# Optimization experiments

Measured on AMD Instinct MI355X. Metric: run time of the kernel, lower is better.

The kernel has to match this reference:

```python
import jax, jax.numpy as jnp
import numpy as np

N = 262144          # pixels (512x512 image)
F = 2               # in_features (x, y)
K = 13              # num_frequencies
H = 256             # dim_hidden
OUT = 3             # out_features (RGB)
TILES = [1, 4, 16, 64, 256]   # prod(tile_dims[i]) per layer
PE_DIM = F + 2 * F * K        # 54


def setup_inputs() -> dict:
    key = jax.random.key(0)
    ks = jax.random.split(key, 2 * len(TILES) + 3)
    inp = {"coords": jax.random.uniform(ks[0], (N, F), dtype=jnp.float32)}
    d_in = PE_DIM
    for i, t in enumerate(TILES):
        # kaiming-uniform-like scale; biases init to zero as in the module
        bound = float(np.sqrt(6.0 / d_in))
        inp[f"w{i}"] = jax.random.uniform(ks[1 + i], (t, d_in, H), dtype=jnp.float32,
                                           minval=-bound, maxval=bound)
        inp[f"b{i}"] = jnp.zeros((H,), dtype=jnp.float32)
        d_in = H
    bound = float(np.sqrt(6.0 / H))
    inp["w_last"] = jax.random.uniform(ks[-1], (OUT, H), dtype=jnp.float32,
                                        minval=-bound, maxval=bound)
    inp["b_last"] = jnp.zeros((OUT,), dtype=jnp.float32)
    return inp


def _pos_enc(coords):
    # NeRF positional encoding, concat order: coords, then for each freq i,
    # for each feature j: sin(2^i * pi * c_j), cos(2^i * pi * c_j)
    freqs = (2.0 ** jnp.arange(K, dtype=jnp.float32)) * np.pi      # [K]
    ang = coords[:, None, :] * freqs[None, :, None]                # [N, K, F]
    enc = jnp.stack([jnp.sin(ang), jnp.cos(ang)], axis=-1)         # [N, K, F, 2]
    enc = enc.reshape(coords.shape[0], 2 * K * F)
    return jnp.concatenate([coords, enc], axis=-1)                 # [N, PE_DIM]


def reference(coords, w0, b0, w1, b1, w2, b2, w3, b3, w4, b4, w_last, b_last):
    x = _pos_enc(coords)                                           # [N, 54]
    for w, b in ((w0, b0), (w1, b1), (w2, b2), (w3, b3), (w4, b4)):
        t = w.shape[0]
        x = x.reshape(t, -1, x.shape[-1])                          # [T, N/T, d_in]
        x = jnp.einsum('tnd,tdo->tno', x, w) + b                   # per-tile GEMM
        x = jnp.where(x > 0, x, 0.2 * x)                           # LeakyReLU(0.2)
    x = x.reshape(-1, H)                                           # [N, H]
    return x @ w_last.T + b_last                                   # [N, OUT]
```

## Files before the change

### kernel.cpp

```cpp
#include <hip/hip_runtime.h>
#include <stdint.h>

typedef uint32_t u32;
typedef short s16x8 __attribute__((ext_vector_type(8)));
typedef float f32x16 __attribute__((ext_vector_type(16)));
typedef u32 u32x2 __attribute__((ext_vector_type(2)));
typedef u32 u32x4 __attribute__((ext_vector_type(4)));

#define NPIX   262144
#define HD     256

#define FTHR      512
#define PXB       128
#define NBLK      (NPIX / PXB)
#define ACT_LDS   65536

#define B0_OFF  0u
#define B1_OFF  32768u
#define B2_OFF  557056u
#define B3_OFF  2654208u
#define B4_OFF  11042816u
#define BH_OFF  44597248u
#define BLOB_TOTAL 44613632u
#define F_W1 2048u
#define F_W2 34816u
#define F_W3 165888u
#define F_W4 690176u
#define F_WH 2787328u
#define F_END 2788352u

#define ACT_BYTES  131072
#define WBUF_BYTES 16384
#define FB_LDS     (ACT_BYTES + 2 * WBUF_BYTES)

__device__ __forceinline__ u32 bfpair(float a, float b) {
    u32 ua = __builtin_bit_cast(u32, a);
    u32 ub = __builtin_bit_cast(u32, b);
    ua = (ua + 0x7FFFu + ((ua >> 16) & 1u)) >> 16;
    ub = (ub + 0x7FFFu + ((ub >> 16) & 1u)) >> 16;
    return ua | (ub << 16);
}
__device__ __forceinline__ u32 act_off(int row, int colByte) {
    return (u32)((row << 9) + (colByte ^ ((row & 31) << 4)));
}
__device__ __forceinline__ u32 w_off32(int col, int kByte) {
    return (u32)((col << 6) + (kByte ^ (((col >> 1) & 3) << 4)));
}

extern "C" __global__ __launch_bounds__(256)
void loe_prepass(const float* __restrict__ w0, const float* __restrict__ w1,
                 const float* __restrict__ w2, const float* __restrict__ w3,
                 const float* __restrict__ w4, const float* __restrict__ wl,
                 char* __restrict__ ws)
{
    const u32 f = blockIdx.x * 256 + threadIdx.x;
    if (f >= F_END) return;
    float v[8];
    char* dst;
    if (f < F_W1) {
        const u32 kk = f >> 9, fb = (f >> 6) & 7, lane = f & 63;
        const u32 l31 = lane & 31, lhi = lane >> 5;
        const u32 k0 = kk * 16 + lhi * 8, col = fb * 32 + l31;
        #pragma unroll
        for (int j = 0; j < 8; ++j)
            v[j] = (k0 + j < 54) ? w0[(k0 + j) * HD + col] : 0.0f;
        dst = ws + B0_OFF + (size_t)f * 16;
    } else if (f < F_WH) {
        const float* W; size_t boff; u32 fl;
        if (f < F_W2)      { W = w1; boff = B1_OFF; fl = f - F_W1; }
        else if (f < F_W3) { W = w2; boff = B2_OFF; fl = f - F_W2; }
        else if (f < F_W4) { W = w3; boff = B3_OFF; fl = f - F_W3; }
        else               { W = w4; boff = B4_OFF; fl = f - F_W4; }
        const u32 t = fl >> 13, c = fl & 8191;
        const u32 kk = c >> 9, fb = (c >> 6) & 7, lane = c & 63;
        const u32 l31 = lane & 31, lhi = lane >> 5;
        const u32 k0 = kk * 16 + lhi * 8, col = fb * 32 + l31;
        const float* src = W + (size_t)t * 65536 + (size_t)k0 * HD + col;
        #pragma unroll
        for (int j = 0; j < 8; ++j) v[j] = src[(size_t)j * HD];
        dst = ws + boff + (size_t)fl * 16;
    } else {
        const u32 fl = f - F_WH;
        const u32 kk = fl >> 6, lane = fl & 63;
        const u32 l31 = lane & 31, lhi = lane >> 5;
        const u32 k0 = kk * 16 + lhi * 8;
        #pragma unroll
        for (int j = 0; j < 8; ++j)
            v[j] = (l31 < 3) ? wl[l31 * HD + k0 + j] : 0.0f;
        dst = ws + BH_OFF + (size_t)fl * 16;
    }
    u32x4 pk;
    pk.x = bfpair(v[0], v[1]); pk.y = bfpair(v[2], v[3]);
    pk.z = bfpair(v[4], v[5]); pk.w = bfpair(v[6], v[7]);
    *reinterpret_cast<u32x4*>(dst) = pk;
}

extern "C" __global__ __launch_bounds__(FTHR, 4)
void loe_fused_pre(const float* __restrict__ coords,
                   const float* __restrict__ b0, const float* __restrict__ b1,
                   const float* __restrict__ b2, const float* __restrict__ b3,
                   const float* __restrict__ b4, const float* __restrict__ bl,
                   const char* __restrict__ blob,
                   float* __restrict__ out)
{
    extern __shared__ char lds[];

    const int tid  = threadIdx.x;
    const int lane = tid & 63;
    const int wv   = tid >> 6;
    const int l31  = lane & 31;
    const int lhi  = lane >> 5;

    const int bid  = (int)blockIdx.x;
    const int pb   = ((bid & 7) << 8) | (bid >> 3);
    const int pix0 = pb << 7;

    {
        const int p = tid >> 2;
        const int h = tid & 3;
        const float2 c2 = reinterpret_cast<const float2*>(coords)[pix0 + p];
        const float cf[2] = {c2.x, c2.y};
        #pragma unroll
        for (int u = 0; u < 16; u += 2) {
            float v[2];
            #pragma unroll
            for (int q = 0; q < 2; ++q) {
                const int c = h * 16 + u + q;
                float val;
                if (c < 2) val = cf[c];
                else if (c - 2 >= 52) val = 0.0f;
                else {
                    const int e = c - 2;
                    const float a = cf[(e >> 1) & 1] * (float)(1 << (e >> 2));
                    val = (e & 1) ? cospif(a) : sinpif(a);
                }
                v[q] = val;
            }
            *reinterpret_cast<u32*>(lds + act_off(p, (h * 16 + u) * 2)) = bfpair(v[0], v[1]);
        }
    }

    f32x16 acc[4];
    const u32 swz = (u32)(l31 << 4);
    u32 abase[4];
    #pragma unroll
    for (int pt = 0; pt < 4; ++pt) abase[pt] = (u32)((pt * 32 + l31) << 9);

    auto init_acc = [&](const float* Bias) {
        #pragma unroll
        for (int q = 0; q < 4; ++q) {
            const float4 bv = *reinterpret_cast<const float4*>(Bias + wv * 32 + q * 8 + lhi * 4);
            #pragma unroll
            for (int pt = 0; pt < 4; ++pt) {
                acc[pt][q * 4 + 0] = bv.x; acc[pt][q * 4 + 1] = bv.y;
                acc[pt][q * 4 + 2] = bv.z; acc[pt][q * 4 + 3] = bv.w;
            }
        }
    };

    auto epilogue = [&]() {
        #pragma unroll
        for (int q = 0; q < 4; ++q) {
            const int oc0 = wv * 32 + q * 8 + lhi * 4;
            #pragma unroll
            for (int pt = 0; pt < 4; ++pt) {
                float x[4];
                #pragma unroll
                for (int j = 0; j < 4; ++j) {
                    const float v = acc[pt][q * 4 + j];
                    x[j] = fmaxf(v, 0.2f * v);
                }
                u32x2 wo;
                wo.x = bfpair(x[0], x[1]);
                wo.y = bfpair(x[2], x[3]);
                *reinterpret_cast<u32x2*>(lds + act_off(pt * 32 + l31, oc0 * 2)) = wo;
            }
        }
    };

    auto run_layer = [&](int KK, const char* wbase, const float* Bias) {
        init_acc(Bias);
        __syncthreads();
        const char* f0 = wbase + (size_t)wv * 1024 + (size_t)lane * 16;
        u32x4 wA = *reinterpret_cast<const u32x4*>(f0);
        u32x4 wB = *reinterpret_cast<const u32x4*>(f0 + 8192);
        #pragma unroll 4
        for (int kk = 0; kk < KK; kk += 2) {
            const int n2 = (kk + 2 < KK) ? kk + 2 : kk;
            const int n3 = (kk + 3 < KK) ? kk + 3 : KK - 1;
            const u32x4 nA = *reinterpret_cast<const u32x4*>(f0 + (size_t)n2 * 8192);
            const u32x4 nB = *reinterpret_cast<const u32x4*>(f0 + (size_t)n3 * 8192);
            {
                const u32 cb = (u32)(kk * 32 + lhi * 16) ^ swz;
                s16x8 af[4];
                #pragma unroll
                for (int pt = 0; pt < 4; ++pt)
                    af[pt] = *reinterpret_cast<const s16x8*>(lds + abase[pt] + cb);
                const s16x8 a = __builtin_bit_cast(s16x8, wA);
                #pragma unroll
                for (int pt = 0; pt < 4; ++pt)
                    acc[pt] = __builtin_amdgcn_mfma_f32_32x32x16_bf16(a, af[pt], acc[pt], 0, 0, 0);
            }
            {
                const u32 cb = (u32)((kk + 1) * 32 + lhi * 16) ^ swz;
                s16x8 af[4];
                #pragma unroll
                for (int pt = 0; pt < 4; ++pt)
                    af[pt] = *reinterpret_cast<const s16x8*>(lds + abase[pt] + cb);
                const s16x8 a = __builtin_bit_cast(s16x8, wB);
                #pragma unroll
                for (int pt = 0; pt < 4; ++pt)
                    acc[pt] = __builtin_amdgcn_mfma_f32_32x32x16_bf16(a, af[pt], acc[pt], 0, 0, 0);
            }
            wA = nA; wB = nB;
        }
        __syncthreads();
        epilogue();
    };

    const char* b0p = blob + B0_OFF;
    const char* b1p = blob + B1_OFF + (size_t)(pb >> 9) * 131072;
    const char* b2p = blob + B2_OFF + (size_t)(pb >> 7) * 131072;
    const char* b3p = blob + B3_OFF + (size_t)(pb >> 5) * 131072;
    const char* b4p = blob + B4_OFF + (size_t)(pb >> 3) * 131072;
    const char* bHp = blob + BH_OFF;

    run_layer(4,  b0p, b0);
    run_layer(16, b1p, b1);
    run_layer(16, b2p, b2);
    run_layer(16, b3p, b3);
    run_layer(16, b4p, b4);

    __syncthreads();
    if (wv < 4) {
        f32x16 a;
        #pragma unroll
        for (int r = 0; r < 16; ++r) a[r] = 0.0f;
        const u32 hrow = (u32)((wv * 32 + l31) << 9);
        #pragma unroll 4
        for (int kk = 0; kk < 16; ++kk) {
            const u32x4 wh = *reinterpret_cast<const u32x4*>(bHp + (size_t)kk * 1024 + (size_t)lane * 16);
            const u32 cb = (u32)(kk * 32 + lhi * 16) ^ swz;
            const s16x8 af = *reinterpret_cast<const s16x8*>(lds + hrow + cb);
            a = __builtin_amdgcn_mfma_f32_32x32x16_bf16(__builtin_bit_cast(s16x8, wh), af, a, 0, 0, 0);
        }
        if (lhi == 0) {
            const int p = pix0 + wv * 32 + l31;
            out[p * 3 + 0] = a[0] + bl[0];
            out[p * 3 + 1] = a[1] + bl[1];
            out[p * 3 + 2] = a[2] + bl[2];
        }
    }
}

extern "C" __global__ __launch_bounds__(512, 2)
void loe_fused_fb(const float* __restrict__ coords,
                  const float* __restrict__ w0, const float* __restrict__ b0,
                  const float* __restrict__ w1, const float* __restrict__ b1,
                  const float* __restrict__ w2, const float* __restrict__ b2,
                  const float* __restrict__ w3, const float* __restrict__ b3,
                  const float* __restrict__ w4, const float* __restrict__ b4,
                  const float* __restrict__ wl, const float* __restrict__ bl,
                  float* __restrict__ out)
{
    extern __shared__ char lds[];
    const int tid  = threadIdx.x;
    const int lane = tid & 63;
    const int wv   = tid >> 6;
    const int wr   = wv >> 2;
    const int wc   = wv & 3;
    const int l31  = lane & 31;
    const int lhi  = lane >> 5;
    const int bid  = (int)blockIdx.x;
    const int pb   = ((bid & 7) << 7) | (bid >> 3);
    const int pix0 = pb << 8;
    const int scol = tid & 255;
    const int kh   = tid >> 8;

    float st[16];
    auto load_plain = [&](const float* W, int s) {
        const float* src = W + (size_t)(s * 32 + kh * 16) * HD + scol;
        #pragma unroll
        for (int j = 0; j < 16; ++j) st[j] = src[(size_t)j * HD];
    };
    auto load_guard = [&](const float* W, int s) {
        #pragma unroll
        for (int j = 0; j < 16; ++j) {
            const int k = s * 32 + kh * 16 + j;
            st[j] = (k < 54) ? W[k * HD + scol] : 0.0f;
        }
    };
    load_guard(w0, 0);
    {
        const int p = tid >> 1;
        const int h = tid & 1;
        const float2 c2 = reinterpret_cast<const float2*>(coords)[pix0 + p];
        const float cf[2] = {c2.x, c2.y};
        #pragma unroll
        for (int u = 0; u < 32; u += 2) {
            float v[2];
            #pragma unroll
            for (int q = 0; q < 2; ++q) {
                const int c = h * 32 + u + q;
                float val;
                if (c < 2) val = cf[c];
                else if (c - 2 >= 52) val = 0.0f;
                else {
                    const int e = c - 2;
                    const float a = cf[(e >> 1) & 1] * (float)(1 << (e >> 2));
                    val = (e & 1) ? cospif(a) : sinpif(a);
                }
                v[q] = val;
            }
            *reinterpret_cast<u32*>(lds + act_off(p, (h * 32 + u) * 2)) = bfpair(v[0], v[1]);
        }
    }
    f32x16 acc[4][2];
    int g = 0;
    auto epilogue = [&](const float* Bias) {
        #pragma unroll
        for (int ct = 0; ct < 2; ++ct)
            #pragma unroll
            for (int q = 0; q < 4; ++q) {
                const int oc0 = wc * 64 + ct * 32 + q * 8 + lhi * 4;
                const float4 bv = *reinterpret_cast<const float4*>(Bias + oc0);
                const float bj[4] = {bv.x, bv.y, bv.z, bv.w};
                #pragma unroll
                for (int pt = 0; pt < 4; ++pt) {
                    const int p = wr * 128 + pt * 32 + l31;
                    float x[4];
                    #pragma unroll
                    for (int j = 0; j < 4; ++j) {
                        float v = acc[pt][ct][q * 4 + j] + bj[j];
                        x[j] = (v > 0.0f) ? v : 0.2f * v;
                    }
                    u32x2 wv2;
                    wv2.x = bfpair(x[0], x[1]);
                    wv2.y = bfpair(x[2], x[3]);
                    *reinterpret_cast<u32x2*>(lds + act_off(p, oc0 * 2)) = wv2;
                }
            }
    };
    auto run_layer = [&](int S, const float* Wcur, const float* Wnext,
                         const float* Bias, bool guard) {
        #pragma unroll
        for (int pt = 0; pt < 4; ++pt)
            #pragma unroll
            for (int ct = 0; ct < 2; ++ct)
                #pragma unroll
                for (int r = 0; r < 16; ++r) acc[pt][ct][r] = 0.0f;
        for (int s = 0; s < S; ++s) {
            char* wbw = lds + ACT_BYTES + ((g & 1) ? WBUF_BYTES : 0);
            u32x4 pk0, pk1;
            pk0.x = bfpair(st[0], st[1]);   pk0.y = bfpair(st[2], st[3]);
            pk0.z = bfpair(st[4], st[5]);   pk0.w = bfpair(st[6], st[7]);
            pk1.x = bfpair(st[8], st[9]);   pk1.y = bfpair(st[10], st[11]);
            pk1.z = bfpair(st[12], st[13]); pk1.w = bfpair(st[14], st[15]);
            *reinterpret_cast<u32x4*>(wbw + w_off32(scol, kh * 32))      = pk0;
            *reinterpret_cast<u32x4*>(wbw + w_off32(scol, kh * 32 + 16)) = pk1;
            if (s + 1 < S) { if (guard) load_guard(Wcur, s + 1); else load_plain(Wcur, s + 1); }
            else if (Wnext) load_plain(Wnext, 0);
            __syncthreads();
            #pragma unroll
            for (int kt = 0; kt < 2; ++kt) {
                const int kb = kt * 32 + lhi * 16;
                s16x8 wf[2], af[4];
                #pragma unroll
                for (int ct = 0; ct < 2; ++ct)
                    wf[ct] = *reinterpret_cast<const s16x8*>(wbw + w_off32(wc * 64 + ct * 32 + l31, kb));
                #pragma unroll
                for (int pt = 0; pt < 4; ++pt)
                    af[pt] = *reinterpret_cast<const s16x8*>(lds + act_off(wr * 128 + pt * 32 + l31, s * 64 + kb));
                #pragma unroll
                for (int pt = 0; pt < 4; ++pt)
                    #pragma unroll
                    for (int ct = 0; ct < 2; ++ct)
                        acc[pt][ct] = __builtin_amdgcn_mfma_f32_32x32x16_bf16(wf[ct], af[pt], acc[pt][ct], 0, 0, 0);
            }
            ++g;
            __syncthreads();
        }
        epilogue(Bias);
        __syncthreads();
    };
    const float* w1t = w1 + (size_t)(pb >> 8) * 65536;
    const float* w2t = w2 + (size_t)(pb >> 6) * 65536;
    const float* w3t = w3 + (size_t)(pb >> 4) * 65536;
    const float* w4t = w4 + (size_t)(pb >> 2) * 65536;
    __syncthreads();
    run_layer(2, w0,  w1t, b0, true);
    run_layer(8, w1t, w2t, b1, false);
    run_layer(8, w2t, w3t, b2, false);
    run_layer(8, w3t, w4t, b3, false);
    run_layer(8, w4t, nullptr, b4, false);
    char* hw = lds + ACT_BYTES;
    #pragma unroll
    for (int rep = 0; rep < 2; ++rep) {
        const int task = rep * 512 + tid;
        const int col  = task & 31;
        const int kg   = task >> 5;
        float v[8];
        #pragma unroll
        for (int j = 0; j < 8; ++j)
            v[j] = (col < 3) ? wl[col * HD + kg * 8 + j] : 0.0f;
        u32x4 pk;
        pk.x = bfpair(v[0], v[1]); pk.y = bfpair(v[2], v[3]);
        pk.z = bfpair(v[4], v[5]); pk.w = bfpair(v[6], v[7]);
        *reinterpret_cast<u32x4*>(hw + col * 512 + ((kg * 16) ^ ((col & 7) << 4))) = pk;
    }
    __syncthreads();
    {
        f32x16 a;
        #pragma unroll
        for (int r = 0; r < 16; ++r) a[r] = 0.0f;
        #pragma unroll
        for (int kt = 0; kt < 16; ++kt) {
            const int kb = kt * 32 + lhi * 16;
            s16x8 wf = *reinterpret_cast<const s16x8*>(hw + l31 * 512 + (kb ^ ((l31 & 7) << 4)));
            s16x8 af = *reinterpret_cast<const s16x8*>(lds + act_off(wv * 32 + l31, kb));
            a = __builtin_amdgcn_mfma_f32_32x32x16_bf16(wf, af, a, 0, 0, 0);
        }
        if (lhi == 0) {
            const int p = pix0 + wv * 32 + l31;
            out[p * 3 + 0] = a[0] + bl[0];
            out[p * 3 + 1] = a[1] + bl[1];
            out[p * 3 + 2] = a[2] + bl[2];
        }
    }
}

extern "C" void kernel_launch(void* const* d_in, const int* in_sizes, int n_in,
                              void* d_out, int out_size, void* d_ws, size_t ws_size,
                              hipStream_t stream) {
    (void)in_sizes; (void)n_in; (void)out_size;
    const float* coords = (const float*)d_in[0];
    const float* w0 = (const float*)d_in[1];  const float* b0 = (const float*)d_in[2];
    const float* w1 = (const float*)d_in[3];  const float* b1 = (const float*)d_in[4];
    const float* w2 = (const float*)d_in[5];  const float* b2 = (const float*)d_in[6];
    const float* w3 = (const float*)d_in[7];  const float* b3 = (const float*)d_in[8];
    const float* w4 = (const float*)d_in[9];  const float* b4 = (const float*)d_in[10];
    const float* wl = (const float*)d_in[11]; const float* bl = (const float*)d_in[12];
    float* out = (float*)d_out;

    if (ws_size >= (size_t)BLOB_TOTAL) {
        (void)hipFuncSetAttribute((const void*)loe_fused_pre,
                                  hipFuncAttributeMaxDynamicSharedMemorySize, ACT_LDS);
        loe_prepass<<<dim3((F_END + 255) / 256), dim3(256), 0, stream>>>(
            w0, w1, w2, w3, w4, wl, (char*)d_ws);
        loe_fused_pre<<<dim3(NBLK), dim3(FTHR), ACT_LDS, stream>>>(
            coords, b0, b1, b2, b3, b4, bl, (const char*)d_ws, out);
    } else {
        (void)hipFuncSetAttribute((const void*)loe_fused_fb,
                                  hipFuncAttributeMaxDynamicSharedMemorySize, FB_LDS);
        loe_fused_fb<<<dim3(NPIX / 256), dim3(512), FB_LDS, stream>>>(
            coords, w0, b0, w1, b1, w2, b2, w3, b3, w4, b4, wl, bl, out);
    }
}
```

Baseline: 191.8 us.

## Prefetch weight fragments four deep and across layer boundaries

Replaces the two-deep weight prefetch with a four-register rotating prefetch and fully unrolls the K loop. The next layer's first four weight fragments are loaded during the current layer's tail, and the first layer's fragments are issued before positional encoding. This hides global/L2 latency at layer starts and across barriers, at the cost of more VGPRs and code size.

```diff
diff --git a/kernel.cpp b/kernel.cpp
--- a/kernel.cpp
+++ b/kernel.cpp
@@ -115,6 +115,21 @@
     const int pb   = ((bid & 7) << 8) | (bid >> 3);
     const int pix0 = pb << 7;
 
+    const size_t fragoff = (size_t)wv * 1024 + (size_t)lane * 16;
+    auto ldfrag = [&](const char* base, int chunk) -> u32x4 {
+        return *reinterpret_cast<const u32x4*>(base + (size_t)chunk * 8192 + fragoff);
+    };
+
+    const char* b0p = blob + B0_OFF;
+    const char* b1p = blob + B1_OFF + (size_t)(pb >> 9) * 131072;
+    const char* b2p = blob + B2_OFF + (size_t)(pb >> 7) * 131072;
+    const char* b3p = blob + B3_OFF + (size_t)(pb >> 5) * 131072;
+    const char* b4p = blob + B4_OFF + (size_t)(pb >> 3) * 131072;
+    const char* bHp = blob + BH_OFF;
+
+    u32x4 wr0 = ldfrag(b0p, 0), wr1 = ldfrag(b0p, 1),
+          wr2 = ldfrag(b0p, 2), wr3 = ldfrag(b0p, 3);
+
     {
         const int p = tid >> 2;
         const int h = tid & 3;
@@ -178,58 +193,37 @@
         }
     };
 
-    auto run_layer = [&](int KK, const char* wbase, const float* Bias) {
+    auto proc = [&](const u32x4& w, int chunk) {
+        const u32 cb = (u32)(chunk * 32 + lhi * 16) ^ swz;
+        s16x8 af[4];
+        #pragma unroll
+        for (int pt = 0; pt < 4; ++pt)
+            af[pt] = *reinterpret_cast<const s16x8*>(lds + abase[pt] + cb);
+        const s16x8 a = __builtin_bit_cast(s16x8, w);
+        #pragma unroll
+        for (int pt = 0; pt < 4; ++pt)
+            acc[pt] = __builtin_amdgcn_mfma_f32_32x32x16_bf16(a, af[pt], acc[pt], 0, 0, 0);
+    };
+
+    auto run_layer = [&](int KK, const char* cur, const char* nxt, const float* Bias) {
         init_acc(Bias);
         __syncthreads();
-        const char* f0 = wbase + (size_t)wv * 1024 + (size_t)lane * 16;
-        u32x4 wA = *reinterpret_cast<const u32x4*>(f0);
-        u32x4 wB = *reinterpret_cast<const u32x4*>(f0 + 8192);
-        #pragma unroll 4
-        for (int kk = 0; kk < KK; kk += 2) {
-            const int n2 = (kk + 2 < KK) ? kk + 2 : kk;
-            const int n3 = (kk + 3 < KK) ? kk + 3 : KK - 1;
-            const u32x4 nA = *reinterpret_cast<const u32x4*>(f0 + (size_t)n2 * 8192);
-            const u32x4 nB = *reinterpret_cast<const u32x4*>(f0 + (size_t)n3 * 8192);
-            {
-                const u32 cb = (u32)(kk * 32 + lhi * 16) ^ swz;
-                s16x8 af[4];
-                #pragma unroll
-                for (int pt = 0; pt < 4; ++pt)
-                    af[pt] = *reinterpret_cast<const s16x8*>(lds + abase[pt] + cb);
-                const s16x8 a = __builtin_bit_cast(s16x8, wA);
-                #pragma unroll
-                for (int pt = 0; pt < 4; ++pt)
-                    acc[pt] = __builtin_amdgcn_mfma_f32_32x32x16_bf16(a, af[pt], acc[pt], 0, 0, 0);
-            }
-            {
-                const u32 cb = (u32)((kk + 1) * 32 + lhi * 16) ^ swz;
-                s16x8 af[4];
-                #pragma unroll
-                for (int pt = 0; pt < 4; ++pt)
-                    af[pt] = *reinterpret_cast<const s16x8*>(lds + abase[pt] + cb);
-                const s16x8 a = __builtin_bit_cast(s16x8, wB);
-                #pragma unroll
-                for (int pt = 0; pt < 4; ++pt)
-                    acc[pt] = __builtin_amdgcn_mfma_f32_32x32x16_bf16(a, af[pt], acc[pt], 0, 0, 0);
-            }
-            wA = nA; wB = nB;
+        #pragma unroll
+        for (int kk = 0; kk < KK; kk += 4) {
+            proc(wr0, kk + 0); wr0 = (kk + 4 < KK) ? ldfrag(cur, kk + 4) : ldfrag(nxt, 0);
+            proc(wr1, kk + 1); wr1 = (kk + 5 < KK) ? ldfrag(cur, kk + 5) : ldfrag(nxt, 1);
+            proc(wr2, kk + 2); wr2 = (kk + 6 < KK) ? ldfrag(cur, kk + 6) : ldfrag(nxt, 2);
+            proc(wr3, kk + 3); wr3 = (kk + 7 < KK) ? ldfrag(cur, kk + 7) : ldfrag(nxt, 3);
         }
         __syncthreads();
         epilogue();
     };
 
-    const char* b0p = blob + B0_OFF;
-    const char* b1p = blob + B1_OFF + (size_t)(pb >> 9) * 131072;
-    const char* b2p = blob + B2_OFF + (size_t)(pb >> 7) * 131072;
-    const char* b3p = blob + B3_OFF + (size_t)(pb >> 5) * 131072;
-    const char* b4p = blob + B4_OFF + (size_t)(pb >> 3) * 131072;
-    const char* bHp = blob + BH_OFF;
-
-    run_layer(4,  b0p, b0);
-    run_layer(16, b1p, b1);
-    run_layer(16, b2p, b2);
-    run_layer(16, b3p, b3);
-    run_layer(16, b4p, b4);
+    run_layer(4,  b0p, b1p, b0);
+    run_layer(16, b1p, b2p, b1);
+    run_layer(16, b2p, b3p, b2);
+    run_layer(16, b3p, b4p, b3);
+    run_layer(16, b4p, b4p, b4);
 
     __syncthreads();
     if (wv < 4) {
```

New measurement: 182.0 us. -5.1%, faster.
